# Kernel tuning notes

Measured on AMD Instinct MI355X. Metric: run time of the kernel, lower is better.

Reference implementation:

```python
import jax, jax.numpy as jnp
import numpy as np

EMB = 768
HEADS = 12
HEAD_DIM = EMB // HEADS  # 64
SCALE = 1.0 / float(np.sqrt(EMB))  # NOTE: source divides by sqrt(emb_size), not sqrt(head_dim)


def setup_inputs() -> dict:
    key = jax.random.key(0)
    k_x, k_wqkv, k_bqkv, k_wp, k_bp = jax.random.split(key, 5)
    b, n = 4, 2048
    x = jax.random.normal(k_x, (b, n, EMB), dtype=jnp.float32)
    # torch Linear default init ~ U(-1/sqrt(in), 1/sqrt(in)); scale doesn't matter for correctness baseline
    lim = 1.0 / np.sqrt(EMB)
    W_qkv = jax.random.uniform(k_wqkv, (EMB, 3 * EMB), minval=-lim, maxval=lim, dtype=jnp.float32)
    b_qkv = jax.random.uniform(k_bqkv, (3 * EMB,), minval=-lim, maxval=lim, dtype=jnp.float32)
    W_proj = jax.random.uniform(k_wp, (EMB, EMB), minval=-lim, maxval=lim, dtype=jnp.float32)
    b_proj = jax.random.uniform(k_bp, (EMB,), minval=-lim, maxval=lim, dtype=jnp.float32)
    return {"x": x, "W_qkv": W_qkv, "b_qkv": b_qkv, "W_proj": W_proj, "b_proj": b_proj}


def reference(x, W_qkv, b_qkv, W_proj, b_proj):
    b, n, _ = x.shape
    qkv = x @ W_qkv + b_qkv                              # [b, n, 3*emb]
    # rearrange 'b n (h d qkv) -> qkv b h n d' : qkv is the innermost split
    qkv = qkv.reshape(b, n, HEADS, HEAD_DIM, 3)
    qkv = jnp.transpose(qkv, (4, 0, 2, 1, 3))            # [3, b, h, n, d]
    q, k, v = qkv[0], qkv[1], qkv[2]
    att = jnp.einsum('bhnd,bhmd->bhnm', q, k) * SCALE    # [b, h, n, n]
    att = jax.nn.softmax(att, axis=-1)
    # dropout is identity at inference
    out = jnp.einsum('bhnm,bhmd->bhnd', att, v)          # [b, h, n, d]
    out = jnp.transpose(out, (0, 2, 1, 3)).reshape(b, n, EMB)  # 'b h n d -> b n (h d)'
    return out @ W_proj + b_proj
```

## Files before the change

kernel.cpp:

```cpp
#include <hip/hip_runtime.h>
#include <math.h>

typedef _Float16 f16x8 __attribute__((ext_vector_type(8)));
typedef _Float16 f16x4 __attribute__((ext_vector_type(4)));
typedef float f32x4 __attribute__((ext_vector_type(4)));
typedef unsigned int uint32;
typedef unsigned short ushort16;

static constexpr int EMB_ = 768;
static constexpr int NH_ = 12;
static constexpr int HD_ = 64;
static constexpr int SEQ_ = 2048;
static constexpr int B_ = 4;
static constexpr float QSCALE_ = 0.036084391824351615f * 1.4426950408889634f;

__device__ __forceinline__ void gload_lds16(const void* g, void* l) {
    __builtin_amdgcn_global_load_lds((const __attribute__((address_space(1))) void*)g,
                                     (__attribute__((address_space(3))) void*)l,
                                     16, 0, 0);
}

__global__ __launch_bounds__(256)
void prep_k(const float* __restrict__ W0, _Float16* __restrict__ Wt0,
            const float* __restrict__ W1, _Float16* __restrict__ Wt1,
            const float* __restrict__ x, _Float16* __restrict__ xh,
            const float* __restrict__ bq, float* __restrict__ bqP,
            int C0, int C1, int n4)
{
    const int tid = threadIdx.x;
    if (blockIdx.z == 2) {
        if (blockIdx.y == 0 && blockIdx.x < 9) {
            const int c = blockIdx.x * 256 + tid;
            const int h = c / 192, rem = c - h * 192;
            const int d = rem / 3, s = rem - d * 3;
            bqP[s * 768 + h * 64 + d] = bq[c];
        }
        const int stride = 72 * 24 * 256;
        for (int i = (blockIdx.y * 72 + blockIdx.x) * 256 + tid; i < n4; i += stride) {
            float4 v = ((const float4*)x)[i];
            f16x4 o = {(_Float16)v.x, (_Float16)v.y, (_Float16)v.z, (_Float16)v.w};
            ((f16x4*)xh)[i] = o;
        }
        return;
    }
    const float* W; _Float16* Wt; int C;
    if (blockIdx.z == 0) { W = W0; Wt = Wt0; C = C0; }
    else                 { W = W1; Wt = Wt1; C = C1; }
    const int c0 = blockIdx.x * 32;
    if (c0 >= C) return;
    const int r0 = blockIdx.y * 32;
    __shared__ float ls[32][33];
    const int tc = tid & 31, tr = tid >> 5;
    const bool perm = (blockIdx.z == 0);
#pragma unroll
    for (int i = 0; i < 4; ++i)
        ls[tr + 8 * i][tc] = W[(size_t)(r0 + tr + 8 * i) * C + c0 + tc];
    __syncthreads();
#pragma unroll
    for (int i = 0; i < 4; ++i) {
        const int c = c0 + tr + 8 * i;
        int cp = c;
        if (perm) {
            const int h = c / 192, rem = c - h * 192;
            const int d = rem / 3, s = rem - d * 3;
            cp = s * 768 + h * 64 + d;
        }
        Wt[(size_t)cp * EMB_ + r0 + tc] = (_Float16)ls[tc][tr + 8 * i];
    }
}

template<int EPI>
__global__ __launch_bounds__(256, 2)
void gemm16(const _Float16* __restrict__ A, const _Float16* __restrict__ Bt,
            const float* __restrict__ bias, float* __restrict__ outF,
            _Float16* __restrict__ hq, _Float16* __restrict__ hk,
            _Float16* __restrict__ hv,
            int M, int N, int K)
{
    __shared__ __align__(16) _Float16 As[128 * 64];
    __shared__ __align__(16) _Float16 Bs[128 * 64];

    const int tid  = threadIdx.x;
    const int lane = tid & 63;
    const int w    = tid >> 6;
    const int txm  = lane & 15, g = lane >> 4;
    const int wr   = w >> 1, wc = w & 1;
    const int m0   = blockIdx.y * 128, n0 = blockIdx.x * 128;
    const int nk   = K >> 6;

    const int sr  = lane >> 3;
    const int scX = (((lane & 7) ^ sr) << 3);
    const _Float16* gA[4]; const _Float16* gB[4];
    _Float16* lA[4]; _Float16* lB[4];
#pragma unroll
    for (int i = 0; i < 4; ++i) {
        const int row = w * 32 + 8 * i;
        gA[i] = A  + (size_t)(m0 + row + sr) * K + scX;
        gB[i] = Bt + (size_t)(n0 + row + sr) * K + scX;
        lA[i] = As + row * 64 + lane * 8;
        lB[i] = Bs + row * 64 + lane * 8;
    }

    f32x4 acc[4][4];
#pragma unroll
    for (int i = 0; i < 4; ++i)
#pragma unroll
        for (int j = 0; j < 4; ++j) acc[i][j] = (f32x4){0.f, 0.f, 0.f, 0.f};

    const int fsw = txm & 7;

    for (int kt = 0; kt < nk; ++kt) {
        __syncthreads();
#pragma unroll
        for (int i = 0; i < 4; ++i) gload_lds16(gA[i] + kt * 64, lA[i]);
#pragma unroll
        for (int i = 0; i < 4; ++i) gload_lds16(gB[i] + kt * 64, lB[i]);
        __syncthreads();

#pragma unroll
        for (int kh = 0; kh < 2; ++kh) {
            const int coff = ((4 * kh + g) ^ fsw) << 3;
            f16x8 af[4], bf[4];
#pragma unroll
            for (int i = 0; i < 4; ++i)
                af[i] = *(const f16x8*)&As[(wr * 64 + 16 * i + txm) * 64 + coff];
#pragma unroll
            for (int j = 0; j < 4; ++j)
                bf[j] = *(const f16x8*)&Bs[(wc * 64 + 16 * j + txm) * 64 + coff];
#pragma unroll
            for (int i = 0; i < 4; ++i)
#pragma unroll
                for (int j = 0; j < 4; ++j)
                    acc[i][j] = __builtin_amdgcn_mfma_f32_16x16x32_f16(af[i], bf[j], acc[i][j], 0, 0, 0);
        }
    }

    if (EPI == 0) {
        const int s  = (n0 >= 1536) ? 2 : (n0 >= 768 ? 1 : 0);
        _Float16* bse = (s == 0) ? hq : (s == 1) ? hk : hv;
        const float scl = (s == 0) ? QSCALE_ : 1.f;
        const int nb = n0 - s * 768;
#pragma unroll
        for (int i = 0; i < 4; ++i) {
            const int mB = m0 + wr * 64 + 16 * i + 4 * g;
#pragma unroll
            for (int j = 0; j < 4; ++j) {
                const int nc = wc * 64 + 16 * j + txm;
                const float bv = bias[n0 + nc];
                const int np = nb + nc;
                const int h  = np >> 6;
                const int dd = np & 63;
#pragma unroll
                for (int r = 0; r < 4; ++r) {
                    const int mm = mB + r;
                    const int bb = mm >> 11;
                    const int nn = mm & (SEQ_ - 1);
                    const int ddE = (s == 1) ? (dd ^ ((nn & 7) * 8)) : dd;
                    bse[(((size_t)(bb * NH_ + h)) * SEQ_ + nn) * HD_ + ddE] =
                        (_Float16)((acc[i][j][r] + bv) * scl);
                }
            }
        }
    } else {
#pragma unroll
        for (int i = 0; i < 4; ++i) {
#pragma unroll
            for (int r = 0; r < 4; ++r) {
                const int mm = m0 + wr * 64 + 16 * i + 4 * g + r;
                float* dst = outF + (size_t)mm * N + n0 + wc * 64 + txm;
#pragma unroll
                for (int j = 0; j < 4; ++j)
                    dst[16 * j] = acc[i][j][r] + bias[n0 + wc * 64 + 16 * j + txm];
            }
        }
    }
}

__global__ __launch_bounds__(256, 3)
void attn_k(const _Float16* __restrict__ Qb, const _Float16* __restrict__ Kb,
            const _Float16* __restrict__ Vb, _Float16* __restrict__ Out)
{
    __shared__ __align__(16) _Float16 Ks[2][64][64];
    __shared__ __align__(16) _Float16 Vs[2][64][72];

    const int tid  = threadIdx.x;
    const int lane = tid & 63;
    const int wv   = tid >> 6;
    const int txm  = lane & 15;
    const int g    = lane >> 4;

    const int lin  = blockIdx.x;
    const int slot = lin >> 3;
    const int bh   = (lin & 7) + 8 * (slot >> 4);
    const int q0   = (slot & 15) << 7;
    const int bb   = bh / NH_;
    const int hh   = bh - bb * NH_;

    const _Float16* KpB = Kb + (size_t)bh * SEQ_ * HD_;
    const _Float16* VpB = Vb + (size_t)bh * SEQ_ * HD_;

    auto kstage = [&](int buf, int kt) {
        const int c0 = kt << 6;
#pragma unroll
        for (int i = 0; i < 2; ++i)
            gload_lds16(KpB + (size_t)(c0 + 16 * wv + 8 * i) * HD_ + lane * 8,
                        &Ks[buf][16 * wv + 8 * i][0] + lane * 8);
    };
    kstage(0, 0);

    f16x8 qf[2][2];
#pragma unroll
    for (int s = 0; s < 2; ++s)
#pragma unroll
        for (int kh = 0; kh < 2; ++kh)
            qf[s][kh] = *(const f16x8*)(Qb +
                ((size_t)bh * SEQ_ + q0 + 32 * wv + 16 * s + txm) * HD_ + 32 * kh + 8 * g);

    const int vc = (tid & 31) << 1;
    const int vd = (tid >> 5) << 3;
    const int swz = (txm & 7) * 8;

    f32x4 o[2][4];
#pragma unroll
    for (int s = 0; s < 2; ++s)
#pragma unroll
        for (int dt = 0; dt < 4; ++dt) o[s][dt] = (f32x4){0.f, 0.f, 0.f, 0.f};
    float li[2] = {0.f, 0.f};

    uint4 va = *(const uint4*)(VpB + (size_t)vc * HD_ + vd);
    uint4 vb = *(const uint4*)(VpB + (size_t)(vc + 1) * HD_ + vd);

    constexpr int NT = SEQ_ / 64;
    for (int kt = 0; kt < NT; ++kt) {
        const int buf = kt & 1;
        {
            const ushort16* pa = (const ushort16*)&va;
            const ushort16* pb = (const ushort16*)&vb;
#pragma unroll
            for (int j = 0; j < 8; ++j) {
                uint32 wrd = (uint32)pa[j] | ((uint32)pb[j] << 16);
                *(uint32*)&Vs[buf][vd + j][vc] = wrd;
            }
        }
        __syncthreads();

        if (kt + 1 < NT) {
            kstage(buf ^ 1, kt + 1);
            const int c0n = (kt + 1) << 6;
            va = *(const uint4*)(VpB + (size_t)(c0n + vc) * HD_ + vd);
            vb = *(const uint4*)(VpB + (size_t)(c0n + vc + 1) * HD_ + vd);
        }

        f16x8 kf[4][2];
#pragma unroll
        for (int ct = 0; ct < 4; ++ct)
#pragma unroll
            for (int kh = 0; kh < 2; ++kh)
                kf[ct][kh] = *(const f16x8*)&Ks[buf][16 * ct + txm][(32 * kh + 8 * g) ^ swz];

        f32x4 st[2][4];
#pragma unroll
        for (int s = 0; s < 2; ++s)
#pragma unroll
            for (int ct = 0; ct < 4; ++ct) {
                f32x4 a = (f32x4){0.f, 0.f, 0.f, 0.f};
                a = __builtin_amdgcn_mfma_f32_16x16x32_f16(kf[ct][0], qf[s][0], a, 0, 0, 0);
                a = __builtin_amdgcn_mfma_f32_16x16x32_f16(kf[ct][1], qf[s][1], a, 0, 0, 0);
                st[s][ct] = a;
            }

        f16x4 vf[4][4];
#pragma unroll
        for (int dt = 0; dt < 4; ++dt)
#pragma unroll
            for (int ct = 0; ct < 4; ++ct)
                vf[dt][ct] = *(const f16x4*)&Vs[buf][16 * dt + txm][16 * ct + 4 * g];

#pragma unroll
        for (int s = 0; s < 2; ++s) {
            f16x4 pb4[4];
#pragma unroll
            for (int ct = 0; ct < 4; ++ct) {
                float p0 = __builtin_amdgcn_exp2f(st[s][ct][0]);
                float p1 = __builtin_amdgcn_exp2f(st[s][ct][1]);
                float p2 = __builtin_amdgcn_exp2f(st[s][ct][2]);
                float p3 = __builtin_amdgcn_exp2f(st[s][ct][3]);
                li[s] += (p0 + p1) + (p2 + p3);
                pb4[ct] = (f16x4){(_Float16)p0, (_Float16)p1, (_Float16)p2, (_Float16)p3};
            }
#pragma unroll
            for (int dt = 0; dt < 4; ++dt) {
                f32x4 a = o[s][dt];
#pragma unroll
                for (int ct = 0; ct < 4; ++ct)
                    a = __builtin_amdgcn_mfma_f32_16x16x16f16(vf[dt][ct], pb4[ct], a, 0, 0, 0);
                o[s][dt] = a;
            }
        }
    }

#pragma unroll
    for (int s = 0; s < 2; ++s) {
        float rs = li[s];
        rs += __shfl_xor(rs, 16);
        rs += __shfl_xor(rs, 32);
        const float inv = 1.f / rs;
        const int q = q0 + 32 * wv + 16 * s + txm;
        _Float16* dst = Out + ((size_t)bb * SEQ_ + q) * EMB_ + hh * HD_;
#pragma unroll
        for (int dt = 0; dt < 4; ++dt) {
            f16x4 pk = {(_Float16)(o[s][dt][0] * inv), (_Float16)(o[s][dt][1] * inv),
                        (_Float16)(o[s][dt][2] * inv), (_Float16)(o[s][dt][3] * inv)};
            *(f16x4*)(dst + 16 * dt + 4 * g) = pk;
        }
    }
}

extern "C" void kernel_launch(void* const* d_in, const int* in_sizes, int n_in,
                              void* d_out, int out_size, void* d_ws, size_t ws_size,
                              hipStream_t stream)
{
    const float* x    = (const float*)d_in[0];
    const float* Wqkv = (const float*)d_in[1];
    const float* bqkv = (const float*)d_in[2];
    const float* Wp   = (const float*)d_in[3];
    const float* bp   = (const float*)d_in[4];
    float* out = (float*)d_out;

    const size_t PER = (size_t)B_ * NH_ * SEQ_ * HD_;
    _Float16* Qh     = (_Float16*)d_ws;
    _Float16* Kh     = Qh + PER;
    _Float16* Vh     = Kh + PER;
    _Float16* xh     = Vh + PER;
    _Float16* WqkvT  = xh + (size_t)B_ * SEQ_ * EMB_;
    _Float16* WprojT = WqkvT + (size_t)EMB_ * 3 * EMB_;
    _Float16* Ah     = WprojT + (size_t)EMB_ * EMB_;
    float*    bqP    = (float*)(Ah + (size_t)B_ * SEQ_ * EMB_);

    const int M = B_ * SEQ_;

    prep_k<<<dim3(72, 24, 3), dim3(256), 0, stream>>>(
        Wqkv, WqkvT, Wp, WprojT, x, xh, bqkv, bqP, 3 * EMB_, EMB_, B_ * SEQ_ * EMB_ / 4);

    gemm16<0><<<dim3(3 * EMB_ / 128, M / 128), dim3(256), 0, stream>>>(
        xh, WqkvT, bqP, nullptr, Qh, Kh, Vh, M, 3 * EMB_, EMB_);

    attn_k<<<dim3((SEQ_ / 128) * B_ * NH_), dim3(256), 0, stream>>>(Qh, Kh, Vh, Ah);

    gemm16<1><<<dim3(EMB_ / 128, M / 128), dim3(256), 0, stream>>>(
        Ah, WprojT, bp, out, nullptr, nullptr, nullptr, M, EMB_, EMB_);
}
```

Before: 222.9 us.

## Switch attention MFMAs to 32x32x16 tiles with permlane32 swap for P fragments

Rewrites the attention inner loop to use 32x32x16 f16 MFMA instructions instead of 16x16 variants for both QK^T and PV. The softmax probabilities are repacked into B-operand layout in registers using v_permlane32_swap, which avoids an LDS round-trip. Fewer, larger MFMAs and fewer LDS fragment reads per tile are meant to raise matrix-core throughput. The cost is higher accumulator register pressure at 3 blocks per CU and a dependence on exact lane-layout correctness.

```diff
diff --git a/kernel.cpp b/kernel.cpp
--- a/kernel.cpp
+++ b/kernel.cpp
@@ -3,8 +3,11 @@
 
 typedef _Float16 f16x8 __attribute__((ext_vector_type(8)));
 typedef _Float16 f16x4 __attribute__((ext_vector_type(4)));
+typedef _Float16 f16x2 __attribute__((ext_vector_type(2)));
 typedef float f32x4 __attribute__((ext_vector_type(4)));
+typedef float f32x16 __attribute__((ext_vector_type(16)));
 typedef unsigned int uint32;
+typedef unsigned int uint32x4 __attribute__((ext_vector_type(4)));
 typedef unsigned short ushort16;
 
 static constexpr int EMB_ = 768;
@@ -186,8 +189,8 @@
     const int tid  = threadIdx.x;
     const int lane = tid & 63;
     const int wv   = tid >> 6;
-    const int txm  = lane & 15;
-    const int g    = lane >> 4;
+    const int l31  = lane & 31;
+    const int h    = lane >> 5;
 
     const int lin  = blockIdx.x;
     const int slot = lin >> 3;
@@ -208,24 +211,24 @@
     };
     kstage(0, 0);
 
-    f16x8 qf[2][2];
-#pragma unroll
-    for (int s = 0; s < 2; ++s)
-#pragma unroll
-        for (int kh = 0; kh < 2; ++kh)
-            qf[s][kh] = *(const f16x8*)(Qb +
-                ((size_t)bh * SEQ_ + q0 + 32 * wv + 16 * s + txm) * HD_ + 32 * kh + 8 * g);
+    f16x8 qf[4];
+    {
+        const _Float16* Qrow = Qb + ((size_t)bh * SEQ_ + q0 + 32 * wv + l31) * HD_;
+#pragma unroll
+        for (int ks = 0; ks < 4; ++ks)
+            qf[ks] = *(const f16x8*)(Qrow + 16 * ks + 8 * h);
+    }
 
     const int vc = (tid & 31) << 1;
     const int vd = (tid >> 5) << 3;
-    const int swz = (txm & 7) * 8;
-
-    f32x4 o[2][4];
-#pragma unroll
-    for (int s = 0; s < 2; ++s)
-#pragma unroll
-        for (int dt = 0; dt < 4; ++dt) o[s][dt] = (f32x4){0.f, 0.f, 0.f, 0.f};
-    float li[2] = {0.f, 0.f};
+    const int swz7 = l31 & 7;
+
+    f32x16 o2[2];
+#pragma unroll
+    for (int dt2 = 0; dt2 < 2; ++dt2)
+#pragma unroll
+        for (int r = 0; r < 16; ++r) o2[dt2][r] = 0.f;
+    float li = 0.f;
 
     uint4 va = *(const uint4*)(VpB + (size_t)vc * HD_ + vd);
     uint4 vb = *(const uint4*)(VpB + (size_t)(vc + 1) * HD_ + vd);
@@ -251,69 +254,68 @@
             vb = *(const uint4*)(VpB + (size_t)(c0n + vc + 1) * HD_ + vd);
         }
 
-        f16x8 kf[4][2];
-#pragma unroll
-        for (int ct = 0; ct < 4; ++ct)
-#pragma unroll
-            for (int kh = 0; kh < 2; ++kh)
-                kf[ct][kh] = *(const f16x8*)&Ks[buf][16 * ct + txm][(32 * kh + 8 * g) ^ swz];
-
-        f32x4 st[2][4];
-#pragma unroll
-        for (int s = 0; s < 2; ++s)
-#pragma unroll
-            for (int ct = 0; ct < 4; ++ct) {
-                f32x4 a = (f32x4){0.f, 0.f, 0.f, 0.f};
-                a = __builtin_amdgcn_mfma_f32_16x16x32_f16(kf[ct][0], qf[s][0], a, 0, 0, 0);
-                a = __builtin_amdgcn_mfma_f32_16x16x32_f16(kf[ct][1], qf[s][1], a, 0, 0, 0);
-                st[s][ct] = a;
+        f32x16 st2[2];
+#pragma unroll
+        for (int ct2 = 0; ct2 < 2; ++ct2) {
+#pragma unroll
+            for (int r = 0; r < 16; ++r) st2[ct2][r] = 0.f;
+            f16x8 kf[4];
+            const int crow = 32 * ct2 + l31;
+#pragma unroll
+            for (int ks = 0; ks < 4; ++ks)
+                kf[ks] = *(const f16x8*)&Ks[buf][crow][((2 * ks + h) ^ swz7) << 3];
+#pragma unroll
+            for (int ks = 0; ks < 4; ++ks)
+                st2[ct2] = __builtin_amdgcn_mfma_f32_32x32x16_f16(kf[ks], qf[ks], st2[ct2], 0, 0, 0);
+        }
+
+        f16x8 pfrag[4];
+#pragma unroll
+        for (int ct2 = 0; ct2 < 2; ++ct2) {
+            uint32 w[8];
+#pragma unroll
+            for (int m = 0; m < 8; ++m) {
+                float p0 = __builtin_amdgcn_exp2f(st2[ct2][2 * m]);
+                float p1 = __builtin_amdgcn_exp2f(st2[ct2][2 * m + 1]);
+                li += p0 + p1;
+                f16x2 t = {(_Float16)p0, (_Float16)p1};
+                w[m] = __builtin_bit_cast(uint32, t);
             }
-
-        f16x4 vf[4][4];
-#pragma unroll
-        for (int dt = 0; dt < 4; ++dt)
-#pragma unroll
-            for (int ct = 0; ct < 4; ++ct)
-                vf[dt][ct] = *(const f16x4*)&Vs[buf][16 * dt + txm][16 * ct + 4 * g];
-
-#pragma unroll
-        for (int s = 0; s < 2; ++s) {
-            f16x4 pb4[4];
-#pragma unroll
-            for (int ct = 0; ct < 4; ++ct) {
-                float p0 = __builtin_amdgcn_exp2f(st[s][ct][0]);
-                float p1 = __builtin_amdgcn_exp2f(st[s][ct][1]);
-                float p2 = __builtin_amdgcn_exp2f(st[s][ct][2]);
-                float p3 = __builtin_amdgcn_exp2f(st[s][ct][3]);
-                li[s] += (p0 + p1) + (p2 + p3);
-                pb4[ct] = (f16x4){(_Float16)p0, (_Float16)p1, (_Float16)p2, (_Float16)p3};
-            }
-#pragma unroll
-            for (int dt = 0; dt < 4; ++dt) {
-                f32x4 a = o[s][dt];
-#pragma unroll
-                for (int ct = 0; ct < 4; ++ct)
-                    a = __builtin_amdgcn_mfma_f32_16x16x16f16(vf[dt][ct], pb4[ct], a, 0, 0, 0);
-                o[s][dt] = a;
-            }
-        }
-    }
-
-#pragma unroll
-    for (int s = 0; s < 2; ++s) {
-        float rs = li[s];
-        rs += __shfl_xor(rs, 16);
-        rs += __shfl_xor(rs, 32);
-        const float inv = 1.f / rs;
-        const int q = q0 + 32 * wv + 16 * s + txm;
-        _Float16* dst = Out + ((size_t)bb * SEQ_ + q) * EMB_ + hh * HD_;
-#pragma unroll
-        for (int dt = 0; dt < 4; ++dt) {
-            f16x4 pk = {(_Float16)(o[s][dt][0] * inv), (_Float16)(o[s][dt][1] * inv),
-                        (_Float16)(o[s][dt][2] * inv), (_Float16)(o[s][dt][3] * inv)};
-            *(f16x4*)(dst + 16 * dt + 4 * g) = pk;
-        }
-    }
+            asm("v_permlane32_swap_b32 %0, %1" : "+v"(w[0]), "+v"(w[2]));
+            asm("v_permlane32_swap_b32 %0, %1" : "+v"(w[1]), "+v"(w[3]));
+            asm("v_permlane32_swap_b32 %0, %1" : "+v"(w[4]), "+v"(w[6]));
+            asm("v_permlane32_swap_b32 %0, %1" : "+v"(w[5]), "+v"(w[7]));
+            uint32x4 lo = {w[0], w[1], w[2], w[3]};
+            uint32x4 hi = {w[4], w[5], w[6], w[7]};
+            pfrag[2 * ct2]     = __builtin_bit_cast(f16x8, lo);
+            pfrag[2 * ct2 + 1] = __builtin_bit_cast(f16x8, hi);
+        }
+
+#pragma unroll
+        for (int dt2 = 0; dt2 < 2; ++dt2) {
+            f16x8 vf[4];
+            const int drow = 32 * dt2 + l31;
+#pragma unroll
+            for (int kc = 0; kc < 4; ++kc)
+                vf[kc] = *(const f16x8*)&Vs[buf][drow][16 * kc + 8 * h];
+#pragma unroll
+            for (int kc = 0; kc < 4; ++kc)
+                o2[dt2] = __builtin_amdgcn_mfma_f32_32x32x16_f16(vf[kc], pfrag[kc], o2[dt2], 0, 0, 0);
+        }
+    }
+
+    float rs = li + __shfl_xor(li, 32);
+    const float inv = 1.f / rs;
+    const int q = q0 + 32 * wv + l31;
+    _Float16* dst = Out + ((size_t)bb * SEQ_ + q) * EMB_ + hh * HD_;
+#pragma unroll
+    for (int dt2 = 0; dt2 < 2; ++dt2)
+#pragma unroll
+        for (int r4 = 0; r4 < 4; ++r4) {
+            f16x4 pk = {(_Float16)(o2[dt2][4 * r4 + 0] * inv), (_Float16)(o2[dt2][4 * r4 + 1] * inv),
+                        (_Float16)(o2[dt2][4 * r4 + 2] * inv), (_Float16)(o2[dt2][4 * r4 + 3] * inv)};
+            *(f16x4*)(dst + 32 * dt2 + 8 * r4 + 4 * h) = pk;
+        }
 }
 
 extern "C" void kernel_launch(void* const* d_in, const int* in_sizes, int n_in,
```

After: 210.1 us. 5.7% less time.
